# Kernel tuning notes

Measured on AMD Instinct MI355X. Metric: run time of the kernel, lower is better.

The kernel has to match this reference:

```python
import jax, jax.numpy as jnp
import numpy as np

NEG_INF = -1e9


def setup_inputs() -> dict:
    key = jax.random.key(0)
    ks = jax.random.split(key, 7)
    N, Q, C = 16, 4096, 77
    D, Dc, H, S = 512, 768, 8, 64
    scale = 0.02
    return {
        "query": jax.random.normal(ks[0], (N, Q, D), jnp.float32),
        "context": jax.random.normal(ks[1], (N, C, Dc), jnp.float32),
        "Wq": jax.random.normal(ks[2], (D, H, S), jnp.float32) * scale,
        "Wk": jax.random.normal(ks[3], (Dc, H, S), jnp.float32) * scale,
        "Wv": jax.random.normal(ks[4], (Dc, H, S), jnp.float32) * scale,
        "Wo": jax.random.normal(ks[5], (H, S, D), jnp.float32) * scale,
        "bo": jnp.zeros((D,), jnp.float32),
    }


def reference(query, context, Wq, Wk, Wv, Wo, bo):
    # Projections: split hidden dim into heads.
    q = jnp.einsum('NQD,DHS->NQHS', query, Wq)      # [N,Q,H,S]
    k = jnp.einsum('NCD,DHS->NCHS', context, Wk)    # [N,C,H,S]
    v = jnp.einsum('NCD,DHS->NCHS', context, Wv)    # [N,C,H,S]
    size_per_head = q.shape[-1]
    # Attention scores [N,H,Q,C], scaled by 1/sqrt(S).
    scores = jnp.einsum('NQHS,NCHS->NHQC', q, k) * (size_per_head ** -0.5)
    weights = jax.nn.softmax(scores, axis=3)
    out = jnp.einsum('NHQC,NCHS->NQHS', weights, v)  # [N,Q,H,S]
    # Merge heads back to model dim with output bias.
    return jnp.einsum('NQHS,HSD->NQD', out, Wo) + bo
```

## Files before the change

### kernel.cpp

```cpp
#include <hip/hip_runtime.h>

typedef unsigned short u16;
typedef unsigned int u32;
typedef __bf16 bf16_t;
typedef bf16_t bf16x8 __attribute__((ext_vector_type(8)));
typedef float floatx4 __attribute__((ext_vector_type(4)));

__device__ __forceinline__ float bf2f(u16 h) {
    union { unsigned u; float f; } v;
    v.u = ((unsigned)h) << 16;
    return v.f;
}

__device__ __forceinline__ u16 f2bf(float f) {
    union { float f; unsigned u; } v;
    v.f = f;
    unsigned r = v.u + 0x7fffu + ((v.u >> 16) & 1u);
    return (u16)(r >> 16);
}

typedef __attribute__((address_space(1))) const u32 gu32;
typedef __attribute__((address_space(3))) u32 lu32;
__device__ __forceinline__ void gload16(const void* g, void* l) {
    __builtin_amdgcn_global_load_lds((gu32*)g, (lu32*)l, 16, 0, 0);
}

__global__ void transpose_one(const float* __restrict__ W, u16* __restrict__ Wt,
                              int K, int N) {
    int idx = blockIdx.x * 256 + threadIdx.x;
    if (idx >= K * N) return;
    int nrow = idx / K;
    int k = idx - nrow * K;
    Wt[idx] = f2bf(W[k * N + nrow]);
}

__global__ void transpose_kv(const float* __restrict__ Wk, const float* __restrict__ Wv,
                             u16* __restrict__ Wt) {
    int idx = blockIdx.x * 256 + threadIdx.x;
    if (idx >= 1024 * 768) return;
    int nrow = idx / 768;
    int k = idx - nrow * 768;
    Wt[idx] = f2bf((nrow < 512) ? Wk[k * 512 + nrow] : Wv[k * 512 + (nrow - 512)]);
}

__global__ void transpose_v(const u16* __restrict__ kv, u16* __restrict__ vt) {
    int idx = blockIdx.x * 256 + threadIdx.x;
    if (idx >= 16 * 8 * 64 * 96) return;
    int c  = idx % 96;
    int t1 = idx / 96;
    int s  = t1 & 63;
    int t2 = t1 >> 6;
    int h  = t2 & 7;
    int n  = t2 >> 3;
    u16 val = 0;
    if (c < 77) val = kv[((long)(n * 77 + c)) * 1024 + 512 + h * 64 + s];
    vt[idx] = val;
}

#define TM 128
#define TN 256
#define TK 32

template <bool A_F32, bool OUT_F32>
__global__ __launch_bounds__(512, 4) void gemm_bt(
    const void* __restrict__ A_, const u16* __restrict__ Bt,
    void* __restrict__ C_, const float* __restrict__ bias,
    int M, int K, int N, int ntl2)
{
    constexpr int AB = A_F32 ? TM * TK * 4 : TM * TK * 2;
    constexpr int BB = TN * TK * 2;
    __shared__ __align__(16) char smem[2 * (AB + BB)];

    const int tid  = threadIdx.x;
    const int lane = tid & 63;
    const int wave = tid >> 6;
    const int quad = lane >> 4;
    const int l16  = lane & 15;
    const int wm   = (wave & 1) * 64;
    const int wn   = (wave >> 1) * 64;

    const int nwg = gridDim.x;
    const int wg  = blockIdx.x;
    const int t   = (wg & 7) * (nwg >> 3) + (wg >> 3);
    const long bm = (long)(t >> ntl2) * TM;
    const long bn = (long)(t & ((1 << ntl2) - 1)) * TN;

    const float* Af = (const float*)A_;
    const u16*   Ab = (const u16*)A_;
    const long   Mm1 = (long)M - 1;

    floatx4 acc[4][4] = {};

    auto stage = [&](int b, int k0) {
        char* Abase = smem + b * (AB + BB);
        u16*  Bb    = (u16*)(Abase + AB);
        #pragma unroll
        for (int p = 0; p < 2; ++p) {
            int ch  = p * 512 + tid;
            int row = ch >> 2;
            int pc  = (ch & 3) ^ ((row >> 1) & 3);
            gload16(Bt + (bn + row) * K + k0 + pc * 8,
                    Bb + (p * 512 + wave * 64) * 8);
        }
        if (A_F32) {
            #pragma unroll
            for (int p = 0; p < 2; ++p) {
                int ch  = p * 512 + tid;
                int row = ch >> 3;
                int pcs = (ch & 7) ^ (row & 7);
                long gr = bm + row; if (gr > Mm1) gr = Mm1;
                gload16(Af + gr * K + k0 + pcs * 4,
                        (float*)Abase + (p * 512 + wave * 64) * 4);
            }
        } else {
            int row = tid >> 2;
            int pc  = (tid & 3) ^ ((row >> 1) & 3);
            long gr = bm + row; if (gr > Mm1) gr = Mm1;
            gload16(Ab + gr * K + k0 + pc * 8,
                    (u16*)Abase + (wave * 64) * 8);
        }
    };

    const int nk = K / TK;
    stage(0, 0);

    for (int tt = 0; tt < nk; ++tt) {
        const int cb = tt & 1;
        if (tt + 1 < nk) {
            stage(cb ^ 1, (tt + 1) * TK);
            if (A_F32) asm volatile("s_waitcnt vmcnt(4)" ::: "memory");
            else       asm volatile("s_waitcnt vmcnt(3)" ::: "memory");
        } else {
            asm volatile("s_waitcnt vmcnt(0)" ::: "memory");
        }
        __builtin_amdgcn_s_barrier();
        __builtin_amdgcn_sched_barrier(0);

        const char* Abase = smem + cb * (AB + BB);
        const u16*  Bb    = (const u16*)(Abase + AB);

        bf16x8 af[4], bfr[4];
        #pragma unroll
        for (int i = 0; i < 4; ++i) {
            int row = wm + i * 16 + l16;
            if (A_F32) {
                const char* arow = Abase + (size_t)row * 128;
                int x = row & 7;
                float4 f0 = *(const float4*)(arow + (((quad * 2)     ^ x) * 16));
                float4 f1 = *(const float4*)(arow + (((quad * 2 + 1) ^ x) * 16));
                union { bf16_t h[8]; bf16x8 v; } pk;
                pk.h[0] = (bf16_t)f0.x; pk.h[1] = (bf16_t)f0.y;
                pk.h[2] = (bf16_t)f0.z; pk.h[3] = (bf16_t)f0.w;
                pk.h[4] = (bf16_t)f1.x; pk.h[5] = (bf16_t)f1.y;
                pk.h[6] = (bf16_t)f1.z; pk.h[7] = (bf16_t)f1.w;
                af[i] = pk.v;
            } else {
                int pcs = quad ^ ((row >> 1) & 3);
                af[i] = *(const bf16x8*)((const u16*)Abase + row * 32 + pcs * 8);
            }
        }
        #pragma unroll
        for (int j = 0; j < 4; ++j) {
            int row = wn + j * 16 + l16;
            int pcs = quad ^ ((row >> 1) & 3);
            bfr[j] = *(const bf16x8*)(Bb + row * 32 + pcs * 8);
        }
        #pragma unroll
        for (int i = 0; i < 4; ++i)
            #pragma unroll
            for (int j = 0; j < 4; ++j)
                acc[i][j] = __builtin_amdgcn_mfma_f32_16x16x32_bf16(
                    af[i], bfr[j], acc[i][j], 0, 0, 0);

        __builtin_amdgcn_s_barrier();
    }

    #pragma unroll
    for (int i = 0; i < 4; ++i) {
        #pragma unroll
        for (int r = 0; r < 4; ++r) {
            long row = bm + wm + i * 16 + quad * 4 + r;
            if (row >= M) continue;
            #pragma unroll
            for (int j = 0; j < 4; ++j) {
                long col = bn + wn + j * 16 + l16;
                float val = acc[i][j][r];
                if (bias) val += bias[col];
                if (OUT_F32) ((float*)C_)[row * N + col] = val;
                else         ((u16*)C_)[row * N + col] = f2bf(val);
            }
        }
    }
}

__global__ __launch_bounds__(256) void attn_kernel(
    const u16* __restrict__ qb,
    const u16* __restrict__ kvb,
    const u16* __restrict__ vt,
    u16* __restrict__ ob)
{
    const int QL = 4096, HS = 512;
    const int q0 = blockIdx.x * 256;
    const int h  = blockIdx.y;
    const int n  = blockIdx.z;

    __shared__ u16 sQP[128 * 104];
    __shared__ u16 ks [80 * 72];
    __shared__ u16 vts[64 * 104];

    const int tid  = threadIdx.x;
    const int lane = tid & 63;
    const int wave = tid >> 6;
    const int quad = lane >> 4;
    const int l16  = lane & 15;
    const int wm   = wave * 32;

    const u16* kbase = kvb + (long)n * 77 * 1024 + h * 64;
    for (int v = tid; v < 640; v += 256) {
        int c = v >> 3, g = (v & 7) * 8;
        uint4 val = make_uint4(0, 0, 0, 0);
        if (c < 77) val = *(const uint4*)(kbase + (long)c * 1024 + g);
        *(uint4*)(&ks[c * 72 + g]) = val;
    }
    const u16* vtbase = vt + (long)((n * 8 + h) * 64) * 96;
    for (int v = tid; v < 768; v += 256) {
        int r = v / 12, c8 = v - r * 12;
        *(uint4*)(&vts[r * 104 + c8 * 8]) = *(const uint4*)(vtbase + v * 8);
    }
    __syncthreads();

    const bool v4ok = (l16 < 13);

    for (int it = 0; it < 2; ++it) {
        const long qrow0 = (long)q0 + it * 128;
        const u16* qbase = qb + ((long)n * QL + qrow0) * HS + h * 64;
        u16*       obase = ob + ((long)n * QL + qrow0) * HS + h * 64;

        #pragma unroll
        for (int p = 0; p < 4; ++p) {
            int v = tid + p * 256;
            int r = v >> 3, g = (v & 7) * 8;
            *(uint4*)(&sQP[r * 72 + g]) = *(const uint4*)(qbase + (long)r * HS + g);
        }
        __syncthreads();

        floatx4 accS[2][5] = {};
        #pragma unroll
        for (int kk = 0; kk < 2; ++kk) {
            bf16x8 aq[2], bk[5];
            #pragma unroll
            for (int t = 0; t < 2; ++t)
                aq[t] = *(const bf16x8*)(&sQP[(wm + t * 16 + l16) * 72 + kk * 32 + quad * 8]);
            #pragma unroll
            for (int j = 0; j < 5; ++j)
                bk[j] = *(const bf16x8*)(&ks[(j * 16 + l16) * 72 + kk * 32 + quad * 8]);
            #pragma unroll
            for (int t = 0; t < 2; ++t)
                #pragma unroll
                for (int j = 0; j < 5; ++j)
                    accS[t][j] = __builtin_amdgcn_mfma_f32_16x16x32_bf16(
                        aq[t], bk[j], accS[t][j], 0, 0, 0);
        }

        float pw[2][5][4];
        #pragma unroll
        for (int t = 0; t < 2; ++t) {
            #pragma unroll
            for (int r = 0; r < 4; ++r) {
                float v0 = accS[t][0][r] * 0.125f;
                float v1 = accS[t][1][r] * 0.125f;
                float v2 = accS[t][2][r] * 0.125f;
                float v3 = accS[t][3][r] * 0.125f;
                float v4 = v4ok ? accS[t][4][r] * 0.125f : -1e30f;
                float mx = fmaxf(fmaxf(fmaxf(v0, v1), fmaxf(v2, v3)), v4);
                mx = fmaxf(mx, __shfl_xor(mx, 1));
                mx = fmaxf(mx, __shfl_xor(mx, 2));
                mx = fmaxf(mx, __shfl_xor(mx, 4));
                mx = fmaxf(mx, __shfl_xor(mx, 8));
                float e0 = __expf(v0 - mx), e1 = __expf(v1 - mx);
                float e2 = __expf(v2 - mx), e3 = __expf(v3 - mx);
                float e4 = __expf(v4 - mx);
                float sum = e0 + e1 + e2 + e3 + e4;
                sum += __shfl_xor(sum, 1);
                sum += __shfl_xor(sum, 2);
                sum += __shfl_xor(sum, 4);
                sum += __shfl_xor(sum, 8);
                float inv = 1.f / sum;
                pw[t][0][r] = e0 * inv; pw[t][1][r] = e1 * inv;
                pw[t][2][r] = e2 * inv; pw[t][3][r] = e3 * inv;
                pw[t][4][r] = e4 * inv;
            }
        }
        __syncthreads();

        #pragma unroll
        for (int t = 0; t < 2; ++t) {
            #pragma unroll
            for (int r = 0; r < 4; ++r) {
                int row = wm + t * 16 + quad * 4 + r;
                #pragma unroll
                for (int j = 0; j < 5; ++j)
                    sQP[row * 104 + j * 16 + l16] = f2bf(pw[t][j][r]);
                sQP[row * 104 + 80 + l16] = 0;
            }
        }
        __syncthreads();

        floatx4 accO[2][4] = {};
        #pragma unroll
        for (int kk = 0; kk < 3; ++kk) {
            bf16x8 aw[2], bv[4];
            #pragma unroll
            for (int t = 0; t < 2; ++t)
                aw[t] = *(const bf16x8*)(&sQP[(wm + t * 16 + l16) * 104 + kk * 32 + quad * 8]);
            #pragma unroll
            for (int j = 0; j < 4; ++j)
                bv[j] = *(const bf16x8*)(&vts[(j * 16 + l16) * 104 + kk * 32 + quad * 8]);
            #pragma unroll
            for (int t = 0; t < 2; ++t)
                #pragma unroll
                for (int j = 0; j < 4; ++j)
                    accO[t][j] = __builtin_amdgcn_mfma_f32_16x16x32_bf16(
                        aw[t], bv[j], accO[t][j], 0, 0, 0);
        }

        #pragma unroll
        for (int t = 0; t < 2; ++t)
            #pragma unroll
            for (int j = 0; j < 4; ++j)
                #pragma unroll
                for (int r = 0; r < 4; ++r) {
                    int row = wm + t * 16 + quad * 4 + r;
                    obase[(long)row * HS + j * 16 + l16] = f2bf(accO[t][j][r]);
                }
        __syncthreads();
    }
}

extern "C" void kernel_launch(void* const* d_in, const int* in_sizes, int n_in,
                              void* d_out, int out_size, void* d_ws, size_t ws_size,
                              hipStream_t stream) {
    const float* query   = (const float*)d_in[0];
    const float* context = (const float*)d_in[1];
    const float* Wq      = (const float*)d_in[2];
    const float* Wk      = (const float*)d_in[3];
    const float* Wv      = (const float*)d_in[4];
    const float* Wo      = (const float*)d_in[5];
    const float* bo      = (const float*)d_in[6];
    float* out = (float*)d_out;

    u16* q_ws  = (u16*)d_ws;
    u16* kv_ws = q_ws + 33554432;
    u16* WqT   = kv_ws + 1261568;
    u16* WkvT  = WqT + 262144;
    u16* WoT   = WkvT + 786432;
    u16* vt_ws = WkvT;

    transpose_one<<<(512 * 512 + 255) / 256, 256, 0, stream>>>(Wq, WqT, 512, 512);
    transpose_kv<<<(1024 * 768 + 255) / 256, 256, 0, stream>>>(Wk, Wv, WkvT);
    transpose_one<<<(512 * 512 + 255) / 256, 256, 0, stream>>>(Wo, WoT, 512, 512);

    gemm_bt<true, false><<<dim3(1024), 512, 0, stream>>>(
        (const void*)query, WqT, (void*)q_ws, nullptr, 65536, 512, 512, 1);
    gemm_bt<true, false><<<dim3(40), 512, 0, stream>>>(
        (const void*)context, WkvT, (void*)kv_ws, nullptr, 1232, 768, 1024, 2);
    transpose_v<<<(16 * 8 * 64 * 96 + 255) / 256, 256, 0, stream>>>(kv_ws, vt_ws);
    attn_kernel<<<dim3(16, 8, 16), 256, 0, stream>>>(q_ws, kv_ws, vt_ws, q_ws);
    gemm_bt<false, true><<<dim3(1024), 512, 0, stream>>>(
        (const void*)q_ws, WoT, (void*)out, bo, 65536, 512, 512, 1);
}
```

Before: 419.3 us.

## Pre-convert query to bf16 and use 256x256 tiled GEMM for projections

Adds a separate fp32-to-bf16 conversion pass for the query, staged in the output buffer, and a new 256x256x64 double-buffered MFMA GEMM with XOR-swizzled LDS and async global-to-LDS loads. This kernel replaces the 128x256 GEMM for the Q projection and the output projection. The intent is more data reuse per tile and smaller A-operand traffic in the GEMM. The cost is an extra pass over the query, lower occupancy (2 waves/SIMD bound, 128KB LDS), and half as many workgroups.

```diff
diff --git a/kernel.cpp b/kernel.cpp
--- a/kernel.cpp
+++ b/kernel.cpp
@@ -55,6 +55,139 @@
     u16 val = 0;
     if (c < 77) val = kv[((long)(n * 77 + c)) * 1024 + 512 + h * 64 + s];
     vt[idx] = val;
+}
+
+__global__ void convert_bf16(const float* __restrict__ src, u16* __restrict__ dst,
+                             long n8) {
+    long i = (long)blockIdx.x * blockDim.x + threadIdx.x;
+    const long stride = (long)gridDim.x * blockDim.x;
+    for (; i < n8; i += stride) {
+        float4 f0 = *(const float4*)(src + i * 8);
+        float4 f1 = *(const float4*)(src + i * 8 + 4);
+        union { u16 h[8]; uint4 u; } pk;
+        pk.h[0] = f2bf(f0.x); pk.h[1] = f2bf(f0.y);
+        pk.h[2] = f2bf(f0.z); pk.h[3] = f2bf(f0.w);
+        pk.h[4] = f2bf(f1.x); pk.h[5] = f2bf(f1.y);
+        pk.h[6] = f2bf(f1.z); pk.h[7] = f2bf(f1.w);
+        *(uint4*)(dst + i * 8) = pk.u;
+    }
+}
+
+template <bool OUT_F32>
+__global__ __launch_bounds__(512, 2) void gemm256(
+    const u16* __restrict__ A, const u16* __restrict__ Bt,
+    void* __restrict__ C_, const float* __restrict__ bias,
+    int M, int K, int N, int ntl2)
+{
+    __shared__ u16 As[2][256 * 64];
+    __shared__ u16 Bs[2][256 * 64];
+
+    const int tid  = threadIdx.x;
+    const int lane = tid & 63;
+    const int wave = tid >> 6;
+    const int quad = lane >> 4;
+    const int l16  = lane & 15;
+    const int wr   = wave & 1;
+    const int wc   = wave >> 1;
+
+    const int nwg = gridDim.x;
+    const int wg  = blockIdx.x;
+    const int t   = (wg & 7) * (nwg >> 3) + (wg >> 3);
+    const long bm = (long)(t >> ntl2) * 256;
+    const long bn = (long)(t & ((1 << ntl2) - 1)) * 256;
+
+    floatx4 acc[8][4] = {};
+
+    auto stage = [&](int b, int k0) {
+        #pragma unroll
+        for (int p = 0; p < 4; ++p) {
+            int ch = p * 512 + tid;
+            int r  = ch >> 3;
+            int cs = (ch & 7) ^ (r & 7);
+            gload16(A + (bm + r) * K + k0 + cs * 8,
+                    &As[b][(p * 512 + wave * 64) * 8]);
+        }
+        #pragma unroll
+        for (int p = 0; p < 4; ++p) {
+            int ch = p * 512 + tid;
+            int r  = ch >> 3;
+            int cs = (ch & 7) ^ (r & 7);
+            gload16(Bt + (bn + r) * K + k0 + cs * 8,
+                    &Bs[b][(p * 512 + wave * 64) * 8]);
+        }
+    };
+
+    const int nk = K >> 6;
+    stage(0, 0);
+    asm volatile("s_waitcnt vmcnt(0)" ::: "memory");
+    __builtin_amdgcn_s_barrier();
+
+    for (int tt = 0; tt < nk; ++tt) {
+        const int cb = tt & 1;
+        const u16* Ab = As[cb];
+        const u16* Bb = Bs[cb];
+
+        bf16x8 bfr[4][2];
+
+        #pragma unroll
+        for (int p = 0; p < 4; ++p) {
+            bf16x8 af[2][2];
+            #pragma unroll
+            for (int ii = 0; ii < 2; ++ii) {
+                int row = wr * 128 + (p * 2 + ii) * 16 + l16;
+                #pragma unroll
+                for (int kk = 0; kk < 2; ++kk)
+                    af[ii][kk] = *(const bf16x8*)(
+                        Ab + row * 64 + (((kk * 4) + quad) ^ (row & 7)) * 8);
+            }
+            if (p == 0) {
+                #pragma unroll
+                for (int j = 0; j < 4; ++j) {
+                    int row = wc * 64 + j * 16 + l16;
+                    #pragma unroll
+                    for (int kk = 0; kk < 2; ++kk)
+                        bfr[j][kk] = *(const bf16x8*)(
+                            Bb + row * 64 + (((kk * 4) + quad) ^ (row & 7)) * 8);
+                }
+                if (tt + 1 < nk) stage(cb ^ 1, (tt + 1) << 6);
+            }
+            asm volatile("s_waitcnt lgkmcnt(0)" ::: "memory");
+            __builtin_amdgcn_sched_barrier(0);
+            __builtin_amdgcn_s_setprio(1);
+            #pragma unroll
+            for (int ii = 0; ii < 2; ++ii)
+                #pragma unroll
+                for (int j = 0; j < 4; ++j)
+                    #pragma unroll
+                    for (int kk = 0; kk < 2; ++kk)
+                        acc[p * 2 + ii][j] = __builtin_amdgcn_mfma_f32_16x16x32_bf16(
+                            af[ii][kk], bfr[j][kk], acc[p * 2 + ii][j], 0, 0, 0);
+            __builtin_amdgcn_s_setprio(0);
+            if (p == 3)
+                asm volatile("s_waitcnt vmcnt(0)" ::: "memory");
+            __builtin_amdgcn_s_barrier();
+        }
+    }
+
+    float bj[4];
+    #pragma unroll
+    for (int j = 0; j < 4; ++j)
+        bj[j] = bias ? bias[bn + wc * 64 + j * 16 + l16] : 0.f;
+
+    #pragma unroll
+    for (int i = 0; i < 8; ++i) {
+        #pragma unroll
+        for (int r = 0; r < 4; ++r) {
+            long row = bm + wr * 128 + i * 16 + quad * 4 + r;
+            #pragma unroll
+            for (int j = 0; j < 4; ++j) {
+                long col = bn + wc * 64 + j * 16 + l16;
+                float val = acc[i][j][r] + bj[j];
+                if (OUT_F32) ((float*)C_)[row * N + col] = val;
+                else         ((u16*)C_)[row * N + col] = f2bf(val);
+            }
+        }
+    }
 }
 
 #define TM 128
@@ -356,16 +489,20 @@
     u16* WoT   = WkvT + 786432;
     u16* vt_ws = WkvT;
 
+    u16* q_bf  = (u16*)d_out;
+
     transpose_one<<<(512 * 512 + 255) / 256, 256, 0, stream>>>(Wq, WqT, 512, 512);
     transpose_kv<<<(1024 * 768 + 255) / 256, 256, 0, stream>>>(Wk, Wv, WkvT);
     transpose_one<<<(512 * 512 + 255) / 256, 256, 0, stream>>>(Wo, WoT, 512, 512);
 
-    gemm_bt<true, false><<<dim3(1024), 512, 0, stream>>>(
-        (const void*)query, WqT, (void*)q_ws, nullptr, 65536, 512, 512, 1);
+    convert_bf16<<<dim3(2048), 256, 0, stream>>>(query, q_bf, 4194304L);
+
+    gemm256<false><<<dim3(512), 512, 0, stream>>>(
+        q_bf, WqT, (void*)q_ws, nullptr, 65536, 512, 512, 1);
     gemm_bt<true, false><<<dim3(40), 512, 0, stream>>>(
         (const void*)context, WkvT, (void*)kv_ws, nullptr, 1232, 768, 1024, 2);
     transpose_v<<<(16 * 8 * 64 * 96 + 255) / 256, 256, 0, stream>>>(kv_ws, vt_ws);
     attn_kernel<<<dim3(16, 8, 16), 256, 0, stream>>>(q_ws, kv_ws, vt_ws, q_ws);
-    gemm_bt<false, true><<<dim3(1024), 512, 0, stream>>>(
-        (const void*)q_ws, WoT, (void*)out, bo, 65536, 512, 512, 1);
-}
+    gemm256<true><<<dim3(512), 512, 0, stream>>>(
+        q_ws, WoT, (void*)out, bo, 65536, 512, 512, 1);
+}
```

New measurement: 436.5 us. 4.1% more time.

## Restructure attention kernel to per-wave 32-row tiles with 512 threads and no inner barriers

Applied to the files above, without the earlier changes.

The attention kernel now runs 8 waves per block, each owning 32 query rows. Q fragments are loaded straight from global memory into registers instead of being staged through shared memory. Softmax probabilities go into a private per-wave LDS slice, which removes the per-iteration __syncthreads barriers and the two-iteration loop. The 1/sqrt(S) scale is folded into the transposed Wq weights, so the per-element multiply on the scores disappears. The costs are more LDS per block and uncoalesced direct global Q loads, and occupancy now depends on the new launch bounds.

```diff
diff --git a/kernel.cpp b/kernel.cpp
--- a/kernel.cpp
+++ b/kernel.cpp
@@ -26,12 +26,12 @@
 }
 
 __global__ void transpose_one(const float* __restrict__ W, u16* __restrict__ Wt,
-                              int K, int N) {
+                              int K, int N, float scale) {
     int idx = blockIdx.x * 256 + threadIdx.x;
     if (idx >= K * N) return;
     int nrow = idx / K;
     int k = idx - nrow * K;
-    Wt[idx] = f2bf(W[k * N + nrow]);
+    Wt[idx] = f2bf(W[k * N + nrow] * scale);
 }
 
 __global__ void transpose_kv(const float* __restrict__ Wk, const float* __restrict__ Wv,
@@ -193,7 +193,7 @@
     }
 }
 
-__global__ __launch_bounds__(256) void attn_kernel(
+__global__ __launch_bounds__(512, 4) void attn_kernel(
     const u16* __restrict__ qb,
     const u16* __restrict__ kvb,
     const u16* __restrict__ vt,
@@ -204,137 +204,117 @@
     const int h  = blockIdx.y;
     const int n  = blockIdx.z;
 
-    __shared__ u16 sQP[128 * 104];
     __shared__ u16 ks [80 * 72];
     __shared__ u16 vts[64 * 104];
+    __shared__ u16 pS [8][32 * 104];
 
     const int tid  = threadIdx.x;
     const int lane = tid & 63;
     const int wave = tid >> 6;
     const int quad = lane >> 4;
     const int l16  = lane & 15;
-    const int wm   = wave * 32;
+
+    const long qrow = (long)n * QL + q0 + wave * 32;
+    bf16x8 aq[2][2];
+    #pragma unroll
+    for (int t = 0; t < 2; ++t)
+        #pragma unroll
+        for (int kk = 0; kk < 2; ++kk)
+            aq[t][kk] = *(const bf16x8*)(
+                qb + (qrow + t * 16 + l16) * HS + h * 64 + kk * 32 + quad * 8);
 
     const u16* kbase = kvb + (long)n * 77 * 1024 + h * 64;
-    for (int v = tid; v < 640; v += 256) {
+    for (int v = tid; v < 640; v += 512) {
         int c = v >> 3, g = (v & 7) * 8;
         uint4 val = make_uint4(0, 0, 0, 0);
         if (c < 77) val = *(const uint4*)(kbase + (long)c * 1024 + g);
         *(uint4*)(&ks[c * 72 + g]) = val;
     }
     const u16* vtbase = vt + (long)((n * 8 + h) * 64) * 96;
-    for (int v = tid; v < 768; v += 256) {
+    for (int v = tid; v < 768; v += 512) {
         int r = v / 12, c8 = v - r * 12;
         *(uint4*)(&vts[r * 104 + c8 * 8]) = *(const uint4*)(vtbase + v * 8);
     }
     __syncthreads();
 
+    floatx4 accS[2][5] = {};
+    #pragma unroll
+    for (int kk = 0; kk < 2; ++kk) {
+        bf16x8 bk[5];
+        #pragma unroll
+        for (int j = 0; j < 5; ++j)
+            bk[j] = *(const bf16x8*)(&ks[(j * 16 + l16) * 72 + kk * 32 + quad * 8]);
+        #pragma unroll
+        for (int t = 0; t < 2; ++t)
+            #pragma unroll
+            for (int j = 0; j < 5; ++j)
+                accS[t][j] = __builtin_amdgcn_mfma_f32_16x16x32_bf16(
+                    aq[t][kk], bk[j], accS[t][j], 0, 0, 0);
+    }
+
     const bool v4ok = (l16 < 13);
-
-    for (int it = 0; it < 2; ++it) {
-        const long qrow0 = (long)q0 + it * 128;
-        const u16* qbase = qb + ((long)n * QL + qrow0) * HS + h * 64;
-        u16*       obase = ob + ((long)n * QL + qrow0) * HS + h * 64;
-
-        #pragma unroll
-        for (int p = 0; p < 4; ++p) {
-            int v = tid + p * 256;
-            int r = v >> 3, g = (v & 7) * 8;
-            *(uint4*)(&sQP[r * 72 + g]) = *(const uint4*)(qbase + (long)r * HS + g);
-        }
-        __syncthreads();
-
-        floatx4 accS[2][5] = {};
-        #pragma unroll
-        for (int kk = 0; kk < 2; ++kk) {
-            bf16x8 aq[2], bk[5];
-            #pragma unroll
-            for (int t = 0; t < 2; ++t)
-                aq[t] = *(const bf16x8*)(&sQP[(wm + t * 16 + l16) * 72 + kk * 32 + quad * 8]);
-            #pragma unroll
-            for (int j = 0; j < 5; ++j)
-                bk[j] = *(const bf16x8*)(&ks[(j * 16 + l16) * 72 + kk * 32 + quad * 8]);
-            #pragma unroll
-            for (int t = 0; t < 2; ++t)
-                #pragma unroll
-                for (int j = 0; j < 5; ++j)
-                    accS[t][j] = __builtin_amdgcn_mfma_f32_16x16x32_bf16(
-                        aq[t], bk[j], accS[t][j], 0, 0, 0);
-        }
-
-        float pw[2][5][4];
-        #pragma unroll
-        for (int t = 0; t < 2; ++t) {
+    u16* pw = pS[wave];
+    #pragma unroll
+    for (int t = 0; t < 2; ++t) {
+        #pragma unroll
+        for (int r = 0; r < 4; ++r) {
+            float v0 = accS[t][0][r];
+            float v1 = accS[t][1][r];
+            float v2 = accS[t][2][r];
+            float v3 = accS[t][3][r];
+            float v4 = v4ok ? accS[t][4][r] : -1e30f;
+            float mx = fmaxf(fmaxf(fmaxf(v0, v1), fmaxf(v2, v3)), v4);
+            mx = fmaxf(mx, __shfl_xor(mx, 1));
+            mx = fmaxf(mx, __shfl_xor(mx, 2));
+            mx = fmaxf(mx, __shfl_xor(mx, 4));
+            mx = fmaxf(mx, __shfl_xor(mx, 8));
+            float e0 = __expf(v0 - mx), e1 = __expf(v1 - mx);
+            float e2 = __expf(v2 - mx), e3 = __expf(v3 - mx);
+            float e4 = __expf(v4 - mx);
+            float sum = e0 + e1 + e2 + e3 + e4;
+            sum += __shfl_xor(sum, 1);
+            sum += __shfl_xor(sum, 2);
+            sum += __shfl_xor(sum, 4);
+            sum += __shfl_xor(sum, 8);
+            float inv = 1.f / sum;
+            int row = t * 16 + quad * 4 + r;
+            pw[row * 104 +  0 + l16] = f2bf(e0 * inv);
+            pw[row * 104 + 16 + l16] = f2bf(e1 * inv);
+            pw[row * 104 + 32 + l16] = f2bf(e2 * inv);
+            pw[row * 104 + 48 + l16] = f2bf(e3 * inv);
+            pw[row * 104 + 64 + l16] = f2bf(e4 * inv);
+            pw[row * 104 + 80 + l16] = 0;
+        }
+    }
+
+    floatx4 accO[2][4] = {};
+    #pragma unroll
+    for (int kk = 0; kk < 3; ++kk) {
+        bf16x8 aw[2], bv[4];
+        #pragma unroll
+        for (int t = 0; t < 2; ++t)
+            aw[t] = *(const bf16x8*)(&pw[(t * 16 + l16) * 104 + kk * 32 + quad * 8]);
+        #pragma unroll
+        for (int j = 0; j < 4; ++j)
+            bv[j] = *(const bf16x8*)(&vts[(j * 16 + l16) * 104 + kk * 32 + quad * 8]);
+        #pragma unroll
+        for (int t = 0; t < 2; ++t)
+            #pragma unroll
+            for (int j = 0; j < 4; ++j)
+                accO[t][j] = __builtin_amdgcn_mfma_f32_16x16x32_bf16(
+                    aw[t], bv[j], accO[t][j], 0, 0, 0);
+    }
+
+    u16* obase = ob + qrow * HS + h * 64;
+    #pragma unroll
+    for (int t = 0; t < 2; ++t)
+        #pragma unroll
+        for (int j = 0; j < 4; ++j)
             #pragma unroll
             for (int r = 0; r < 4; ++r) {
-                float v0 = accS[t][0][r] * 0.125f;
-                float v1 = accS[t][1][r] * 0.125f;
-                float v2 = accS[t][2][r] * 0.125f;
-                float v3 = accS[t][3][r] * 0.125f;
-                float v4 = v4ok ? accS[t][4][r] * 0.125f : -1e30f;
-                float mx = fmaxf(fmaxf(fmaxf(v0, v1), fmaxf(v2, v3)), v4);
-                mx = fmaxf(mx, __shfl_xor(mx, 1));
-                mx = fmaxf(mx, __shfl_xor(mx, 2));
-                mx = fmaxf(mx, __shfl_xor(mx, 4));
-                mx = fmaxf(mx, __shfl_xor(mx, 8));
-                float e0 = __expf(v0 - mx), e1 = __expf(v1 - mx);
-                float e2 = __expf(v2 - mx), e3 = __expf(v3 - mx);
-                float e4 = __expf(v4 - mx);
-                float sum = e0 + e1 + e2 + e3 + e4;
-                sum += __shfl_xor(sum, 1);
-                sum += __shfl_xor(sum, 2);
-                sum += __shfl_xor(sum, 4);
-                sum += __shfl_xor(sum, 8);
-                float inv = 1.f / sum;
-                pw[t][0][r] = e0 * inv; pw[t][1][r] = e1 * inv;
-                pw[t][2][r] = e2 * inv; pw[t][3][r] = e3 * inv;
-                pw[t][4][r] = e4 * inv;
+                int row = t * 16 + quad * 4 + r;
+                obase[(long)row * HS + j * 16 + l16] = f2bf(accO[t][j][r]);
             }
-        }
-        __syncthreads();
-
-        #pragma unroll
-        for (int t = 0; t < 2; ++t) {
-            #pragma unroll
-            for (int r = 0; r < 4; ++r) {
-                int row = wm + t * 16 + quad * 4 + r;
-                #pragma unroll
-                for (int j = 0; j < 5; ++j)
-                    sQP[row * 104 + j * 16 + l16] = f2bf(pw[t][j][r]);
-                sQP[row * 104 + 80 + l16] = 0;
-            }
-        }
-        __syncthreads();
-
-        floatx4 accO[2][4] = {};
-        #pragma unroll
-        for (int kk = 0; kk < 3; ++kk) {
-            bf16x8 aw[2], bv[4];
-            #pragma unroll
-            for (int t = 0; t < 2; ++t)
-                aw[t] = *(const bf16x8*)(&sQP[(wm + t * 16 + l16) * 104 + kk * 32 + quad * 8]);
-            #pragma unroll
-            for (int j = 0; j < 4; ++j)
-                bv[j] = *(const bf16x8*)(&vts[(j * 16 + l16) * 104 + kk * 32 + quad * 8]);
-            #pragma unroll
-            for (int t = 0; t < 2; ++t)
-                #pragma unroll
-                for (int j = 0; j < 4; ++j)
-                    accO[t][j] = __builtin_amdgcn_mfma_f32_16x16x32_bf16(
-                        aw[t], bv[j], accO[t][j], 0, 0, 0);
-        }
-
-        #pragma unroll
-        for (int t = 0; t < 2; ++t)
-            #pragma unroll
-            for (int j = 0; j < 4; ++j)
-                #pragma unroll
-                for (int r = 0; r < 4; ++r) {
-                    int row = wm + t * 16 + quad * 4 + r;
-                    obase[(long)row * HS + j * 16 + l16] = f2bf(accO[t][j][r]);
-                }
-        __syncthreads();
-    }
 }
 
 extern "C" void kernel_launch(void* const* d_in, const int* in_sizes, int n_in,
@@ -356,16 +336,16 @@
     u16* WoT   = WkvT + 786432;
     u16* vt_ws = WkvT;
 
-    transpose_one<<<(512 * 512 + 255) / 256, 256, 0, stream>>>(Wq, WqT, 512, 512);
+    transpose_one<<<(512 * 512 + 255) / 256, 256, 0, stream>>>(Wq, WqT, 512, 512, 0.125f);
     transpose_kv<<<(1024 * 768 + 255) / 256, 256, 0, stream>>>(Wk, Wv, WkvT);
-    transpose_one<<<(512 * 512 + 255) / 256, 256, 0, stream>>>(Wo, WoT, 512, 512);
+    transpose_one<<<(512 * 512 + 255) / 256, 256, 0, stream>>>(Wo, WoT, 512, 512, 1.0f);
 
     gemm_bt<true, false><<<dim3(1024), 512, 0, stream>>>(
         (const void*)query, WqT, (void*)q_ws, nullptr, 65536, 512, 512, 1);
     gemm_bt<true, false><<<dim3(40), 512, 0, stream>>>(
         (const void*)context, WkvT, (void*)kv_ws, nullptr, 1232, 768, 1024, 2);
     transpose_v<<<(16 * 8 * 64 * 96 + 255) / 256, 256, 0, stream>>>(kv_ws, vt_ws);
-    attn_kernel<<<dim3(16, 8, 16), 256, 0, stream>>>(q_ws, kv_ws, vt_ws, q_ws);
+    attn_kernel<<<dim3(16, 8, 16), 512, 0, stream>>>(q_ws, kv_ws, vt_ws, q_ws);
     gemm_bt<false, true><<<dim3(1024), 512, 0, stream>>>(
-        (const void*)q_ws, WoT, (void*)out, bo, 65536, 512, 512, 1);
-}
+        q_ws, WoT, (void*)out, bo, 65536, 512, 512, 1);
+}
```

Result: faster. 405.4 us (-3.3%).
